# Kernel optimization log

Measured on AMD Instinct MI355X. Metric: run time of the kernel, lower is better.

The kernel has to match this reference:

```python
import math
import jax, jax.numpy as jnp
import numpy as np

B, DK, N = 16, 512, 2048


def setup_inputs() -> dict:
    key = jax.random.key(0)
    k1, k2, k3, k4, k5 = jax.random.split(key, 5)
    return {
        "src_embedding": jax.random.normal(k1, (B, DK, N), dtype=jnp.float32),
        "tgt_embedding": jax.random.normal(k2, (B, DK, N), dtype=jnp.float32),
        "src": jax.random.normal(k3, (B, 3, N), dtype=jnp.float32),
        "tgt": jax.random.normal(k4, (B, 3, N), dtype=jnp.float32),
        "temperature": jax.random.uniform(k5, (B,), dtype=jnp.float32),
    }


def reference(src_embedding, tgt_embedding, src, tgt, temperature):
    batch, d_k, num_points = src_embedding.shape
    # scores[b, n, m] = <src_emb[b,:,n], tgt_emb[b,:,m]> / sqrt(d_k)
    scores = jnp.einsum("bdn,bdm->bnm", src_embedding, tgt_embedding) / math.sqrt(d_k)
    temp = temperature.reshape(batch, 1, 1)
    scores = jax.nn.softmax(temp * scores, axis=2)  # [B, N, N]

    # src_corr = tgt @ scores^T : soft correspondences in tgt for each src point
    src_corr = jnp.einsum("bdm,bnm->bdn", tgt, scores)  # [B, 3, N]

    src_mean = src.mean(axis=2, keepdims=True)          # [B, 3, 1]
    corr_mean = src_corr.mean(axis=2, keepdims=True)    # [B, 3, 1]

    # Cross-covariance H = src_centered @ src_corr_centered^T  -> [B, 3, 3]
    H = jnp.einsum("bin,bjn->bij", src - src_mean, src_corr - corr_mean)

    # Batched Kabsch via 3x3 SVD (torch.svd: H = u @ diag(s) @ v^T; jnp: H = u @ diag(s) @ vh)
    u, s, vh = jnp.linalg.svd(H)
    v = jnp.swapaxes(vh, -1, -2)
    ut = jnp.swapaxes(u, -1, -2)
    r0 = jnp.matmul(v, ut)
    det = jnp.linalg.det(r0)  # [B]
    ones = jnp.ones_like(det)
    d = jnp.stack([ones, ones, det], axis=-1)  # diag(1, 1, det) per batch
    R = jnp.matmul(v * d[:, None, :], ut)      # v @ diag(d) @ u^T, [B, 3, 3]

    t = jnp.matmul(-R, src_mean) + corr_mean   # [B, 3, 1]
    return R, t.reshape(batch, 3)
```

## Files before the change

kernel.cpp:

```cpp
#include <hip/hip_runtime.h>
#include <math.h>

#define NB 16
#define DKC 512
#define NP 2048
#define BN 128
#define BM 128
#define BK 64
#define NKC (DKC / BK)

typedef __attribute__((ext_vector_type(8))) short sh8;
typedef __attribute__((ext_vector_type(4))) float f32x4;

__global__ __launch_bounds__(512, 2) void attn_moments_mfma(
    const float* __restrict__ src_emb,
    const float* __restrict__ tgt_emb,
    const float* __restrict__ src_pts,
    const float* __restrict__ tgt_pts,
    const float* __restrict__ temperature,
    double* __restrict__ moments)
{
    __shared__ short Qhi[BN * BK];
    __shared__ short Qlo[BN * BK];
    __shared__ short Khi[2][BM * BK];
    __shared__ short Klo[2][BM * BK];
    __shared__ float cw[8][4][16][4];

    const int bid = blockIdx.x;
    const int b = bid >> 4;
    const int nt = bid & 15;
    const int n0 = nt * BN;

    const int tid = threadIdx.x;
    const int lane = tid & 63;
    const int wv = tid >> 6;
    const int wn = (wv >> 2) * 64;
    const int wm = (wv & 3) * 32;
    const int g = lane >> 4;
    const int r15 = lane & 15;

    const float c2 = temperature[b] * (0.044194173824159216f * 1.4426950408889634f);

    float den[4][4], nx[4][4], ny[4][4], nz[4][4];
#pragma unroll
    for (int fr = 0; fr < 4; ++fr)
#pragma unroll
        for (int i = 0; i < 4; ++i) { den[fr][i] = 0.f; nx[fr][i] = 0.f; ny[fr][i] = 0.f; nz[fr][i] = 0.f; }

    const int kg = wv;
    const int srow = lane * 2;
    const size_t ebase = (size_t)b * DKC * NP;
    const float* gq = src_emb + ebase + n0 + srow;
    const float* gk = tgt_emb + ebase + srow;
    const size_t pb3 = (size_t)b * 3 * NP;

    auto stage_tile = [&](const float* gsrc, short* dhi, short* dlo, int kbase) {
        float2 v[8];
#pragma unroll
        for (int j = 0; j < 8; ++j)
            v[j] = *(const float2*)(gsrc + (size_t)(kbase + kg * 8 + j) * NP);
#pragma unroll
        for (int r = 0; r < 2; ++r) {
            const int row = srow + r;
            sh8 H, L;
#pragma unroll
            for (int j = 0; j < 8; ++j) {
                const float x = (r == 0) ? v[j].x : v[j].y;
                const unsigned u = __float_as_uint(x);
                const float lof = x - __uint_as_float(u & 0xffff0000u);
                H[j] = (short)(u >> 16);
                L[j] = (short)(__float_as_uint(lof) >> 16);
            }
            const int unit = row * 8 + (kg ^ (row & 7) ^ ((row >> 3) & 7));
            *(sh8*)(dhi + unit * 8) = H;
            *(sh8*)(dlo + unit * 8) = L;
        }
    };

    for (int pt = 0; pt < NP / (2 * BM); ++pt) {
        const int m0 = pt * (2 * BM);
        f32x4 acc[2][4][2];
#pragma unroll
        for (int t = 0; t < 2; ++t)
#pragma unroll
            for (int fr = 0; fr < 4; ++fr)
#pragma unroll
                for (int mf = 0; mf < 2; ++mf) acc[t][fr][mf] = (f32x4)(0.f);

        for (int kc = 0; kc < NKC; ++kc) {
            const int kb = kc * BK;
            __syncthreads();
            stage_tile(gq,           Qhi,    Qlo,    kb);
            stage_tile(gk + m0,      Khi[0], Klo[0], kb);
            stage_tile(gk + m0 + BM, Khi[1], Klo[1], kb);
            __syncthreads();

#pragma unroll
            for (int ks = 0; ks < 2; ++ks) {
                const int slot = ks * 4 + g;
                sh8 ah[4], al[4];
#pragma unroll
                for (int fr = 0; fr < 4; ++fr) {
                    const int ar = wn + fr * 16 + r15;
                    const int unit = ar * 8 + (slot ^ (ar & 7) ^ ((ar >> 3) & 7));
                    ah[fr] = *(const sh8*)(Qhi + unit * 8);
                    al[fr] = *(const sh8*)(Qlo + unit * 8);
                }
#pragma unroll
                for (int t = 0; t < 2; ++t) {
                    sh8 bh[2], bl[2];
#pragma unroll
                    for (int mf = 0; mf < 2; ++mf) {
                        const int br = wm + mf * 16 + r15;
                        const int unit = br * 8 + (slot ^ (br & 7) ^ ((br >> 3) & 7));
                        bh[mf] = *(const sh8*)(Khi[t] + unit * 8);
                        bl[mf] = *(const sh8*)(Klo[t] + unit * 8);
                    }
#pragma unroll
                    for (int fr = 0; fr < 4; ++fr)
#pragma unroll
                        for (int mf = 0; mf < 2; ++mf) {
                            acc[t][fr][mf] = __builtin_amdgcn_mfma_f32_16x16x32_bf16(ah[fr], bh[mf], acc[t][fr][mf], 0, 0, 0);
                            acc[t][fr][mf] = __builtin_amdgcn_mfma_f32_16x16x32_bf16(ah[fr], bl[mf], acc[t][fr][mf], 0, 0, 0);
                            acc[t][fr][mf] = __builtin_amdgcn_mfma_f32_16x16x32_bf16(al[fr], bh[mf], acc[t][fr][mf], 0, 0, 0);
                        }
                }
            }
        }

#pragma unroll
        for (int t = 0; t < 2; ++t)
#pragma unroll
            for (int mf = 0; mf < 2; ++mf) {
                const int mc = m0 + t * BM + wm + mf * 16 + r15;
                const float t0 = tgt_pts[pb3 + mc];
                const float t1 = tgt_pts[pb3 + NP + mc];
                const float t2 = tgt_pts[pb3 + 2 * NP + mc];
#pragma unroll
                for (int fr = 0; fr < 4; ++fr)
#pragma unroll
                    for (int i = 0; i < 4; ++i) {
                        const float p = exp2f(c2 * acc[t][fr][mf][i]);
                        den[fr][i] += p;
                        nx[fr][i] += p * t0;
                        ny[fr][i] += p * t1;
                        nz[fr][i] += p * t2;
                    }
            }
    }

#pragma unroll
    for (int fr = 0; fr < 4; ++fr)
#pragma unroll
        for (int i = 0; i < 4; ++i) {
#pragma unroll
            for (int off = 1; off <= 8; off <<= 1) {
                den[fr][i] += __shfl_xor(den[fr][i], off);
                nx[fr][i] += __shfl_xor(nx[fr][i], off);
                ny[fr][i] += __shfl_xor(ny[fr][i], off);
                nz[fr][i] += __shfl_xor(nz[fr][i], off);
            }
        }

    __syncthreads();
    if (r15 == 0) {
#pragma unroll
        for (int fr = 0; fr < 4; ++fr)
#pragma unroll
            for (int i = 0; i < 4; ++i) {
                cw[wv][g][fr * 4 + i][0] = den[fr][i];
                cw[wv][g][fr * 4 + i][1] = nx[fr][i];
                cw[wv][g][fr * 4 + i][2] = ny[fr][i];
                cw[wv][g][fr * 4 + i][3] = nz[fr][i];
            }
    }
    __syncthreads();

    if (tid < 128) {
        const int r = tid;
        const int wnIdx = r >> 6;
        const int fi = ((r >> 4) & 3) * 4 + (r & 3);
        const int gg = (r >> 2) & 3;
        float D = 0.f, X = 0.f, Y = 0.f, Z = 0.f;
#pragma unroll
        for (int w = 0; w < 4; ++w) {
            const int wave = wnIdx * 4 + w;
            D += cw[wave][gg][fi][0];
            X += cw[wave][gg][fi][1];
            Y += cw[wave][gg][fi][2];
            Z += cw[wave][gg][fi][3];
        }
        const int n = n0 + r;
        const double inv = 1.0 / (double)D;
        const double c0 = (double)X * inv;
        const double c1 = (double)Y * inv;
        const double c2d = (double)Z * inv;
        const double s0 = (double)src_pts[pb3 + n];
        const double s1 = (double)src_pts[pb3 + NP + n];
        const double s2 = (double)src_pts[pb3 + 2 * NP + n];
        double m15[15];
        m15[0] = s0;  m15[1] = s1;  m15[2] = s2;
        m15[3] = c0;  m15[4] = c1;  m15[5] = c2d;
        m15[6] = s0 * c0;  m15[7] = s0 * c1;  m15[8] = s0 * c2d;
        m15[9] = s1 * c0;  m15[10] = s1 * c1; m15[11] = s1 * c2d;
        m15[12] = s2 * c0; m15[13] = s2 * c1; m15[14] = s2 * c2d;
#pragma unroll
        for (int q = 0; q < 15; ++q)
#pragma unroll
            for (int off = 1; off <= 32; off <<= 1)
                m15[q] += __shfl_xor(m15[q], off);
        if ((tid & 63) == 0) {
            double* mb = moments + b * 15;
#pragma unroll
            for (int q = 0; q < 15; ++q) atomicAdd(&mb[q], m15[q]);
        }
    }
}

__global__ void kabsch_finalize(const double* __restrict__ moments,
                                float* __restrict__ out)
{
    const int b = blockIdx.x;
    if (threadIdx.x != 0) return;
    const double* a = moments + b * 15;

    const double invN = 1.0 / NP;
    const double mus[3] = { a[0] * invN, a[1] * invN, a[2] * invN };
    const double muc[3] = { a[3] * invN, a[4] * invN, a[5] * invN };
    double Hm[3][3];
    for (int i = 0; i < 3; ++i)
        for (int j = 0; j < 3; ++j)
            Hm[i][j] = a[6 + i * 3 + j] - (double)NP * mus[i] * muc[j];

    double A[3][3], V[3][3] = { {1,0,0},{0,1,0},{0,0,1} };
    for (int i = 0; i < 3; ++i)
        for (int j = 0; j < 3; ++j) {
            double s = 0;
            for (int k = 0; k < 3; ++k) s += Hm[k][i] * Hm[k][j];
            A[i][j] = s;
        }
    const int PP[3] = { 0, 0, 1 }, QQ[3] = { 1, 2, 2 };
    for (int sweep = 0; sweep < 20; ++sweep) {
        for (int r = 0; r < 3; ++r) {
            const int p = PP[r], q = QQ[r];
            const double apq = A[p][q];
            if (apq * apq <= 1e-32 * A[p][p] * A[q][q]) continue;
            const double theta = (A[q][q] - A[p][p]) / (2.0 * apq);
            const double tt = (theta >= 0 ? 1.0 : -1.0) / (fabs(theta) + sqrt(1.0 + theta * theta));
            const double c = 1.0 / sqrt(1.0 + tt * tt);
            const double s = tt * c;
            for (int k = 0; k < 3; ++k) {
                const double akp = A[k][p], akq = A[k][q];
                A[k][p] = c * akp - s * akq;
                A[k][q] = s * akp + c * akq;
            }
            for (int k = 0; k < 3; ++k) {
                const double apk = A[p][k], aqk = A[q][k];
                A[p][k] = c * apk - s * aqk;
                A[q][k] = s * apk + c * aqk;
            }
            for (int k = 0; k < 3; ++k) {
                const double vkp = V[k][p], vkq = V[k][q];
                V[k][p] = c * vkp - s * vkq;
                V[k][q] = s * vkp + c * vkq;
            }
        }
    }
    int idx[3] = { 0, 1, 2 };
    for (int i = 0; i < 2; ++i)
        for (int j = i + 1; j < 3; ++j)
            if (A[idx[j]][idx[j]] > A[idx[i]][idx[i]]) { const int t = idx[i]; idx[i] = idx[j]; idx[j] = t; }
    double Vs[3][3], U[3][3];
    for (int j = 0; j < 3; ++j)
        for (int i = 0; i < 3; ++i) Vs[i][j] = V[i][idx[j]];
    for (int j = 0; j < 3; ++j) {
        double hv[3] = { 0, 0, 0 };
        for (int i = 0; i < 3; ++i)
            for (int k = 0; k < 3; ++k) hv[i] += Hm[i][k] * Vs[k][j];
        double s = sqrt(hv[0] * hv[0] + hv[1] * hv[1] + hv[2] * hv[2]);
        s = fmax(s, 1e-300);
        for (int i = 0; i < 3; ++i) U[i][j] = hv[i] / s;
    }
    double R0[3][3];
    for (int i = 0; i < 3; ++i)
        for (int j = 0; j < 3; ++j)
            R0[i][j] = Vs[i][0] * U[j][0] + Vs[i][1] * U[j][1] + Vs[i][2] * U[j][2];
    const double det =
        R0[0][0] * (R0[1][1] * R0[2][2] - R0[1][2] * R0[2][1])
      - R0[0][1] * (R0[1][0] * R0[2][2] - R0[1][2] * R0[2][0])
      + R0[0][2] * (R0[1][0] * R0[2][1] - R0[1][1] * R0[2][0]);
    const double dsg = (det < 0.0) ? -1.0 : 1.0;
    double R[3][3];
    for (int i = 0; i < 3; ++i)
        for (int j = 0; j < 3; ++j)
            R[i][j] = Vs[i][0] * U[j][0] + Vs[i][1] * U[j][1] + dsg * Vs[i][2] * U[j][2];
    for (int i = 0; i < 3; ++i)
        for (int j = 0; j < 3; ++j)
            out[b * 9 + i * 3 + j] = (float)R[i][j];
    for (int i = 0; i < 3; ++i) {
        const double ti = -(R[i][0] * mus[0] + R[i][1] * mus[1] + R[i][2] * mus[2]) + muc[i];
        out[NB * 9 + b * 3 + i] = (float)ti;
    }
}

extern "C" void kernel_launch(void* const* d_in, const int* in_sizes, int n_in,
                              void* d_out, int out_size, void* d_ws, size_t ws_size,
                              hipStream_t stream)
{
    const float* src_emb = (const float*)d_in[0];
    const float* tgt_emb = (const float*)d_in[1];
    const float* src_pts = (const float*)d_in[2];
    const float* tgt_pts = (const float*)d_in[3];
    const float* temp    = (const float*)d_in[4];
    float* out = (float*)d_out;
    double* moments = (double*)d_ws;

    hipMemsetAsync(d_ws, 0, NB * 15 * sizeof(double), stream);
    attn_moments_mfma<<<dim3(NB * 16), dim3(512), 0, stream>>>(
        src_emb, tgt_emb, src_pts, tgt_pts, temp, moments);
    kabsch_finalize<<<dim3(NB), dim3(64), 0, stream>>>(moments, out);
}
```

Before: 473.5 us.

## Prefetch next tile into registers and fuse Kabsch finalize via last-block counter

Flattens the m-tile and k-chunk loops into one step loop. Global loads for the next step are issued into registers while the current tile is converted to bf16 hi/lo and computed, so memory latency overlaps with MFMA work. The separate finalize kernel is removed: the last block per batch, found with an atomic counter, runs the 3x3 Jacobi SVD inline, and the sweep count drops from 20 to 12. This costs more registers for the prefetch buffers, which may hurt occupancy at the two-blocks-per-CU launch bound.

```diff
diff --git a/kernel.cpp b/kernel.cpp
--- a/kernel.cpp
+++ b/kernel.cpp
@@ -7,10 +7,91 @@
 #define BN 128
 #define BM 128
 #define BK 64
-#define NKC (DKC / BK)
+#define NSTEP 64
 
 typedef __attribute__((ext_vector_type(8))) short sh8;
 typedef __attribute__((ext_vector_type(4))) float f32x4;
+
+__device__ void kabsch_body(const double* a, float* out, int b)
+{
+    const double invN = 1.0 / NP;
+    const double mus[3] = { a[0] * invN, a[1] * invN, a[2] * invN };
+    const double muc[3] = { a[3] * invN, a[4] * invN, a[5] * invN };
+    double Hm[3][3];
+    for (int i = 0; i < 3; ++i)
+        for (int j = 0; j < 3; ++j)
+            Hm[i][j] = a[6 + i * 3 + j] - (double)NP * mus[i] * muc[j];
+
+    double A[3][3], V[3][3] = { {1,0,0},{0,1,0},{0,0,1} };
+    for (int i = 0; i < 3; ++i)
+        for (int j = 0; j < 3; ++j) {
+            double s = 0;
+            for (int k = 0; k < 3; ++k) s += Hm[k][i] * Hm[k][j];
+            A[i][j] = s;
+        }
+    const int PP[3] = { 0, 0, 1 }, QQ[3] = { 1, 2, 2 };
+    for (int sweep = 0; sweep < 12; ++sweep) {
+        for (int r = 0; r < 3; ++r) {
+            const int p = PP[r], q = QQ[r];
+            const double apq = A[p][q];
+            if (apq * apq <= 1e-32 * A[p][p] * A[q][q]) continue;
+            const double theta = (A[q][q] - A[p][p]) / (2.0 * apq);
+            const double tt = (theta >= 0 ? 1.0 : -1.0) / (fabs(theta) + sqrt(1.0 + theta * theta));
+            const double c = 1.0 / sqrt(1.0 + tt * tt);
+            const double s = tt * c;
+            for (int k = 0; k < 3; ++k) {
+                const double akp = A[k][p], akq = A[k][q];
+                A[k][p] = c * akp - s * akq;
+                A[k][q] = s * akp + c * akq;
+            }
+            for (int k = 0; k < 3; ++k) {
+                const double apk = A[p][k], aqk = A[q][k];
+                A[p][k] = c * apk - s * aqk;
+                A[q][k] = s * apk + c * aqk;
+            }
+            for (int k = 0; k < 3; ++k) {
+                const double vkp = V[k][p], vkq = V[k][q];
+                V[k][p] = c * vkp - s * vkq;
+                V[k][q] = s * vkp + c * vkq;
+            }
+        }
+    }
+    int idx[3] = { 0, 1, 2 };
+    for (int i = 0; i < 2; ++i)
+        for (int j = i + 1; j < 3; ++j)
+            if (A[idx[j]][idx[j]] > A[idx[i]][idx[i]]) { const int t = idx[i]; idx[i] = idx[j]; idx[j] = t; }
+    double Vs[3][3], U[3][3];
+    for (int j = 0; j < 3; ++j)
+        for (int i = 0; i < 3; ++i) Vs[i][j] = V[i][idx[j]];
+    for (int j = 0; j < 3; ++j) {
+        double hv[3] = { 0, 0, 0 };
+        for (int i = 0; i < 3; ++i)
+            for (int k = 0; k < 3; ++k) hv[i] += Hm[i][k] * Vs[k][j];
+        double s = sqrt(hv[0] * hv[0] + hv[1] * hv[1] + hv[2] * hv[2]);
+        s = fmax(s, 1e-300);
+        for (int i = 0; i < 3; ++i) U[i][j] = hv[i] / s;
+    }
+    double R0[3][3];
+    for (int i = 0; i < 3; ++i)
+        for (int j = 0; j < 3; ++j)
+            R0[i][j] = Vs[i][0] * U[j][0] + Vs[i][1] * U[j][1] + Vs[i][2] * U[j][2];
+    const double det =
+        R0[0][0] * (R0[1][1] * R0[2][2] - R0[1][2] * R0[2][1])
+      - R0[0][1] * (R0[1][0] * R0[2][2] - R0[1][2] * R0[2][0])
+      + R0[0][2] * (R0[1][0] * R0[2][1] - R0[1][1] * R0[2][0]);
+    const double dsg = (det < 0.0) ? -1.0 : 1.0;
+    double R[3][3];
+    for (int i = 0; i < 3; ++i)
+        for (int j = 0; j < 3; ++j)
+            R[i][j] = Vs[i][0] * U[j][0] + Vs[i][1] * U[j][1] + dsg * Vs[i][2] * U[j][2];
+    for (int i = 0; i < 3; ++i)
+        for (int j = 0; j < 3; ++j)
+            out[b * 9 + i * 3 + j] = (float)R[i][j];
+    for (int i = 0; i < 3; ++i) {
+        const double ti = -(R[i][0] * mus[0] + R[i][1] * mus[1] + R[i][2] * mus[2]) + muc[i];
+        out[NB * 9 + b * 3 + i] = (float)ti;
+    }
+}
 
 __global__ __launch_bounds__(512, 2) void attn_moments_mfma(
     const float* __restrict__ src_emb,
@@ -18,7 +99,9 @@
     const float* __restrict__ src_pts,
     const float* __restrict__ tgt_pts,
     const float* __restrict__ temperature,
-    double* __restrict__ moments)
+    double* __restrict__ moments,
+    int* __restrict__ counters,
+    float* __restrict__ out)
 {
     __shared__ short Qhi[BN * BK];
     __shared__ short Qlo[BN * BK];
@@ -54,99 +137,115 @@
     const float* gk = tgt_emb + ebase + srow;
     const size_t pb3 = (size_t)b * 3 * NP;
 
-    auto stage_tile = [&](const float* gsrc, short* dhi, short* dlo, int kbase) {
-        float2 v[8];
-#pragma unroll
-        for (int j = 0; j < 8; ++j)
-            v[j] = *(const float2*)(gsrc + (size_t)(kbase + kg * 8 + j) * NP);
-#pragma unroll
-        for (int r = 0; r < 2; ++r) {
-            const int row = srow + r;
-            sh8 H, L;
-#pragma unroll
-            for (int j = 0; j < 8; ++j) {
-                const float x = (r == 0) ? v[j].x : v[j].y;
-                const unsigned u = __float_as_uint(x);
-                const float lof = x - __uint_as_float(u & 0xffff0000u);
-                H[j] = (short)(u >> 16);
-                L[j] = (short)(__float_as_uint(lof) >> 16);
-            }
-            const int unit = row * 8 + (kg ^ (row & 7) ^ ((row >> 3) & 7));
-            *(sh8*)(dhi + unit * 8) = H;
-            *(sh8*)(dlo + unit * 8) = L;
+    float2 V[3][8];
+    auto issue_loads = [&](int s) {
+        const int kb = (s & 7) * BK;
+        const int mo = (s >> 3) * (2 * BM);
+        const float* g0 = gq + (size_t)(kb + kg * 8) * NP;
+        const float* g1 = gk + mo + (size_t)(kb + kg * 8) * NP;
+#pragma unroll
+        for (int j = 0; j < 8; ++j) {
+            V[0][j] = *(const float2*)(g0 + (size_t)j * NP);
+            V[1][j] = *(const float2*)(g1 + (size_t)j * NP);
+            V[2][j] = *(const float2*)(g1 + BM + (size_t)j * NP);
         }
     };
-
-    for (int pt = 0; pt < NP / (2 * BM); ++pt) {
-        const int m0 = pt * (2 * BM);
-        f32x4 acc[2][4][2];
-#pragma unroll
-        for (int t = 0; t < 2; ++t)
-#pragma unroll
-            for (int fr = 0; fr < 4; ++fr)
-#pragma unroll
-                for (int mf = 0; mf < 2; ++mf) acc[t][fr][mf] = (f32x4)(0.f);
-
-        for (int kc = 0; kc < NKC; ++kc) {
-            const int kb = kc * BK;
-            __syncthreads();
-            stage_tile(gq,           Qhi,    Qlo,    kb);
-            stage_tile(gk + m0,      Khi[0], Klo[0], kb);
-            stage_tile(gk + m0 + BM, Khi[1], Klo[1], kb);
-            __syncthreads();
-
-#pragma unroll
-            for (int ks = 0; ks < 2; ++ks) {
-                const int slot = ks * 4 + g;
-                sh8 ah[4], al[4];
-#pragma unroll
-                for (int fr = 0; fr < 4; ++fr) {
-                    const int ar = wn + fr * 16 + r15;
-                    const int unit = ar * 8 + (slot ^ (ar & 7) ^ ((ar >> 3) & 7));
-                    ah[fr] = *(const sh8*)(Qhi + unit * 8);
-                    al[fr] = *(const sh8*)(Qlo + unit * 8);
+    auto cvt_write = [&]() {
+#pragma unroll
+        for (int t = 0; t < 3; ++t) {
+            short* dhi = (t == 0) ? Qhi : Khi[t - 1];
+            short* dlo = (t == 0) ? Qlo : Klo[t - 1];
+#pragma unroll
+            for (int r = 0; r < 2; ++r) {
+                const int row = srow + r;
+                sh8 H, L;
+#pragma unroll
+                for (int j = 0; j < 8; ++j) {
+                    const float x = (r == 0) ? V[t][j].x : V[t][j].y;
+                    const unsigned u = __float_as_uint(x);
+                    const float lof = x - __uint_as_float(u & 0xffff0000u);
+                    H[j] = (short)(u >> 16);
+                    L[j] = (short)(__float_as_uint(lof) >> 16);
                 }
-#pragma unroll
-                for (int t = 0; t < 2; ++t) {
-                    sh8 bh[2], bl[2];
+                const int unit = row * 8 + (kg ^ (row & 7) ^ ((row >> 3) & 7));
+                *(sh8*)(dhi + unit * 8) = H;
+                *(sh8*)(dlo + unit * 8) = L;
+            }
+        }
+    };
+
+    f32x4 acc[2][4][2];
+    issue_loads(0);
+
+    for (int s = 0; s < NSTEP; ++s) {
+        const int kc = s & 7;
+        if (kc == 0) {
+#pragma unroll
+            for (int t = 0; t < 2; ++t)
+#pragma unroll
+                for (int fr = 0; fr < 4; ++fr)
+#pragma unroll
+                    for (int mf = 0; mf < 2; ++mf) acc[t][fr][mf] = (f32x4)(0.f);
+        }
+        __syncthreads();
+        cvt_write();
+        if (s + 1 < NSTEP) issue_loads(s + 1);
+        __syncthreads();
+
+#pragma unroll
+        for (int ks = 0; ks < 2; ++ks) {
+            const int slot = ks * 4 + g;
+            sh8 ah[4], al[4];
+#pragma unroll
+            for (int fr = 0; fr < 4; ++fr) {
+                const int ar = wn + fr * 16 + r15;
+                const int unit = ar * 8 + (slot ^ (ar & 7) ^ ((ar >> 3) & 7));
+                ah[fr] = *(const sh8*)(Qhi + unit * 8);
+                al[fr] = *(const sh8*)(Qlo + unit * 8);
+            }
+#pragma unroll
+            for (int t = 0; t < 2; ++t) {
+                sh8 bh[2], bl[2];
+#pragma unroll
+                for (int mf = 0; mf < 2; ++mf) {
+                    const int br = wm + mf * 16 + r15;
+                    const int unit = br * 8 + (slot ^ (br & 7) ^ ((br >> 3) & 7));
+                    bh[mf] = *(const sh8*)(Khi[t] + unit * 8);
+                    bl[mf] = *(const sh8*)(Klo[t] + unit * 8);
+                }
+#pragma unroll
+                for (int fr = 0; fr < 4; ++fr)
 #pragma unroll
                     for (int mf = 0; mf < 2; ++mf) {
-                        const int br = wm + mf * 16 + r15;
-                        const int unit = br * 8 + (slot ^ (br & 7) ^ ((br >> 3) & 7));
-                        bh[mf] = *(const sh8*)(Khi[t] + unit * 8);
-                        bl[mf] = *(const sh8*)(Klo[t] + unit * 8);
+                        acc[t][fr][mf] = __builtin_amdgcn_mfma_f32_16x16x32_bf16(ah[fr], bh[mf], acc[t][fr][mf], 0, 0, 0);
+                        acc[t][fr][mf] = __builtin_amdgcn_mfma_f32_16x16x32_bf16(ah[fr], bl[mf], acc[t][fr][mf], 0, 0, 0);
+                        acc[t][fr][mf] = __builtin_amdgcn_mfma_f32_16x16x32_bf16(al[fr], bh[mf], acc[t][fr][mf], 0, 0, 0);
                     }
+            }
+        }
+
+        if (kc == 7) {
+            const int m0 = (s >> 3) * (2 * BM);
+#pragma unroll
+            for (int t = 0; t < 2; ++t)
+#pragma unroll
+                for (int mf = 0; mf < 2; ++mf) {
+                    const int mc = m0 + t * BM + wm + mf * 16 + r15;
+                    const float t0 = tgt_pts[pb3 + mc];
+                    const float t1 = tgt_pts[pb3 + NP + mc];
+                    const float t2 = tgt_pts[pb3 + 2 * NP + mc];
 #pragma unroll
                     for (int fr = 0; fr < 4; ++fr)
 #pragma unroll
-                        for (int mf = 0; mf < 2; ++mf) {
-                            acc[t][fr][mf] = __builtin_amdgcn_mfma_f32_16x16x32_bf16(ah[fr], bh[mf], acc[t][fr][mf], 0, 0, 0);
-                            acc[t][fr][mf] = __builtin_amdgcn_mfma_f32_16x16x32_bf16(ah[fr], bl[mf], acc[t][fr][mf], 0, 0, 0);
-                            acc[t][fr][mf] = __builtin_amdgcn_mfma_f32_16x16x32_bf16(al[fr], bh[mf], acc[t][fr][mf], 0, 0, 0);
+                        for (int i = 0; i < 4; ++i) {
+                            const float p = exp2f(c2 * acc[t][fr][mf][i]);
+                            den[fr][i] += p;
+                            nx[fr][i] += p * t0;
+                            ny[fr][i] += p * t1;
+                            nz[fr][i] += p * t2;
                         }
                 }
-            }
-        }
-
-#pragma unroll
-        for (int t = 0; t < 2; ++t)
-#pragma unroll
-            for (int mf = 0; mf < 2; ++mf) {
-                const int mc = m0 + t * BM + wm + mf * 16 + r15;
-                const float t0 = tgt_pts[pb3 + mc];
-                const float t1 = tgt_pts[pb3 + NP + mc];
-                const float t2 = tgt_pts[pb3 + 2 * NP + mc];
-#pragma unroll
-                for (int fr = 0; fr < 4; ++fr)
-#pragma unroll
-                    for (int i = 0; i < 4; ++i) {
-                        const float p = exp2f(c2 * acc[t][fr][mf][i]);
-                        den[fr][i] += p;
-                        nx[fr][i] += p * t0;
-                        ny[fr][i] += p * t1;
-                        nz[fr][i] += p * t2;
-                    }
-            }
+        }
     }
 
 #pragma unroll
@@ -215,91 +314,21 @@
             for (int q = 0; q < 15; ++q) atomicAdd(&mb[q], m15[q]);
         }
     }
-}
-
-__global__ void kabsch_finalize(const double* __restrict__ moments,
-                                float* __restrict__ out)
-{
-    const int b = blockIdx.x;
-    if (threadIdx.x != 0) return;
-    const double* a = moments + b * 15;
-
-    const double invN = 1.0 / NP;
-    const double mus[3] = { a[0] * invN, a[1] * invN, a[2] * invN };
-    const double muc[3] = { a[3] * invN, a[4] * invN, a[5] * invN };
-    double Hm[3][3];
-    for (int i = 0; i < 3; ++i)
-        for (int j = 0; j < 3; ++j)
-            Hm[i][j] = a[6 + i * 3 + j] - (double)NP * mus[i] * muc[j];
-
-    double A[3][3], V[3][3] = { {1,0,0},{0,1,0},{0,0,1} };
-    for (int i = 0; i < 3; ++i)
-        for (int j = 0; j < 3; ++j) {
-            double s = 0;
-            for (int k = 0; k < 3; ++k) s += Hm[k][i] * Hm[k][j];
-            A[i][j] = s;
-        }
-    const int PP[3] = { 0, 0, 1 }, QQ[3] = { 1, 2, 2 };
-    for (int sweep = 0; sweep < 20; ++sweep) {
-        for (int r = 0; r < 3; ++r) {
-            const int p = PP[r], q = QQ[r];
-            const double apq = A[p][q];
-            if (apq * apq <= 1e-32 * A[p][p] * A[q][q]) continue;
-            const double theta = (A[q][q] - A[p][p]) / (2.0 * apq);
-            const double tt = (theta >= 0 ? 1.0 : -1.0) / (fabs(theta) + sqrt(1.0 + theta * theta));
-            const double c = 1.0 / sqrt(1.0 + tt * tt);
-            const double s = tt * c;
-            for (int k = 0; k < 3; ++k) {
-                const double akp = A[k][p], akq = A[k][q];
-                A[k][p] = c * akp - s * akq;
-                A[k][q] = s * akp + c * akq;
-            }
-            for (int k = 0; k < 3; ++k) {
-                const double apk = A[p][k], aqk = A[q][k];
-                A[p][k] = c * apk - s * aqk;
-                A[q][k] = s * apk + c * aqk;
-            }
-            for (int k = 0; k < 3; ++k) {
-                const double vkp = V[k][p], vkq = V[k][q];
-                V[k][p] = c * vkp - s * vkq;
-                V[k][q] = s * vkp + c * vkq;
-            }
-        }
-    }
-    int idx[3] = { 0, 1, 2 };
-    for (int i = 0; i < 2; ++i)
-        for (int j = i + 1; j < 3; ++j)
-            if (A[idx[j]][idx[j]] > A[idx[i]][idx[i]]) { const int t = idx[i]; idx[i] = idx[j]; idx[j] = t; }
-    double Vs[3][3], U[3][3];
-    for (int j = 0; j < 3; ++j)
-        for (int i = 0; i < 3; ++i) Vs[i][j] = V[i][idx[j]];
-    for (int j = 0; j < 3; ++j) {
-        double hv[3] = { 0, 0, 0 };
-        for (int i = 0; i < 3; ++i)
-            for (int k = 0; k < 3; ++k) hv[i] += Hm[i][k] * Vs[k][j];
-        double s = sqrt(hv[0] * hv[0] + hv[1] * hv[1] + hv[2] * hv[2]);
-        s = fmax(s, 1e-300);
-        for (int i = 0; i < 3; ++i) U[i][j] = hv[i] / s;
-    }
-    double R0[3][3];
-    for (int i = 0; i < 3; ++i)
-        for (int j = 0; j < 3; ++j)
-            R0[i][j] = Vs[i][0] * U[j][0] + Vs[i][1] * U[j][1] + Vs[i][2] * U[j][2];
-    const double det =
-        R0[0][0] * (R0[1][1] * R0[2][2] - R0[1][2] * R0[2][1])
-      - R0[0][1] * (R0[1][0] * R0[2][2] - R0[1][2] * R0[2][0])
-      + R0[0][2] * (R0[1][0] * R0[2][1] - R0[1][1] * R0[2][0]);
-    const double dsg = (det < 0.0) ? -1.0 : 1.0;
-    double R[3][3];
-    for (int i = 0; i < 3; ++i)
-        for (int j = 0; j < 3; ++j)
-            R[i][j] = Vs[i][0] * U[j][0] + Vs[i][1] * U[j][1] + dsg * Vs[i][2] * U[j][2];
-    for (int i = 0; i < 3; ++i)
-        for (int j = 0; j < 3; ++j)
-            out[b * 9 + i * 3 + j] = (float)R[i][j];
-    for (int i = 0; i < 3; ++i) {
-        const double ti = -(R[i][0] * mus[0] + R[i][1] * mus[1] + R[i][2] * mus[2]) + muc[i];
-        out[NB * 9 + b * 3 + i] = (float)ti;
+
+    __syncthreads();
+    if (tid == 0) {
+        __threadfence();
+        const int prev = __hip_atomic_fetch_add(&counters[b], 1, __ATOMIC_ACQ_REL,
+                                                __HIP_MEMORY_SCOPE_AGENT);
+        if (prev == 15 - 1 + 1 - 1 + 1) {  }
+        if (prev == 15) {
+            double a[15];
+            const double* mb = moments + b * 15;
+#pragma unroll
+            for (int q = 0; q < 15; ++q)
+                a[q] = __hip_atomic_load(&mb[q], __ATOMIC_ACQUIRE, __HIP_MEMORY_SCOPE_AGENT);
+            kabsch_body(a, out, b);
+        }
     }
 }
 
@@ -314,9 +343,9 @@
     const float* temp    = (const float*)d_in[4];
     float* out = (float*)d_out;
     double* moments = (double*)d_ws;
-
-    hipMemsetAsync(d_ws, 0, NB * 15 * sizeof(double), stream);
+    int* counters = (int*)((char*)d_ws + NB * 15 * sizeof(double));
+
+    hipMemsetAsync(d_ws, 0, NB * 15 * sizeof(double) + NB * sizeof(int), stream);
     attn_moments_mfma<<<dim3(NB * 16), dim3(512), 0, stream>>>(
-        src_emb, tgt_emb, src_pts, tgt_pts, temp, moments);
-    kabsch_finalize<<<dim3(NB), dim3(64), 0, stream>>>(moments, out);
+        src_emb, tgt_emb, src_pts, tgt_pts, temp, moments, counters, out);
 }
```

After: 534.9 us. +12.9%, slower.
